# Kernel tuning notes

Hardware: AMD Instinct MI355X
Metric: run time of the kernel (lower is better)

Reference implementation:

```python
import jax, jax.numpy as jnp
import numpy as np

B, S, N, C, OUT = 16, 1024, 4096, 768, 256


def setup_inputs() -> dict:
    key = jax.random.key(0)
    k0, k1, k2, k3, k4 = jax.random.split(key, 5)
    seed_xyz = jax.random.normal(k0, (B, S, 3), jnp.float32)   # normalized seed coords
    p_last = jax.random.normal(k1, (B, N, 3), jnp.float32)     # lift3d last-stage coords
    f_last = jax.random.normal(k2, (B, C, N), jnp.float32)     # lift3d last-stage features (channel-first)
    W = jax.random.normal(k3, (OUT, C), jnp.float32) * 0.02    # Conv1d(C, 256, kernel_size=1) weight
    b = jax.random.normal(k4, (OUT,), jnp.float32) * 0.02      # Conv1d bias
    return {"seed_xyz": seed_xyz, "p_last": p_last, "f_last": f_last, "W": W, "b": b}


def reference(seed_xyz, p_last, f_last, W, b):
    # Squared pairwise distances [B,S,N] (argmin invariant to sqrt)
    d2 = (jnp.sum(seed_xyz * seed_xyz, axis=-1, keepdims=True)          # [B,S,1]
          - 2.0 * jnp.einsum('bsd,bnd->bsn', seed_xyz, p_last)          # [B,S,N]
          + jnp.sum(p_last * p_last, axis=-1)[:, None, :])              # [B,1,N]
    idx = jnp.argmin(d2, axis=-1)                                       # [B,S]
    # Gather nearest-neighbor features: [B,C,N] -> [B,C,S]
    gathered = jnp.take_along_axis(f_last, idx[:, None, :], axis=2)
    # 1x1 Conv1d projector: [B,C,S] x [OUT,C] -> [B,OUT,S]
    seed_features = jnp.einsum('bcs,oc->bos', gathered, W) + b[None, :, None]
    return seed_features
```

## Files before the change

### kernel.cpp

```cpp
#include <hip/hip_runtime.h>
#include <stdint.h>

#define B_   16
#define S_   1024
#define N_   4096
#define C_   768
#define OUT_ 256
#define NT_  (C_ / 32)

typedef short bf16x8 __attribute__((ext_vector_type(8)));
typedef short bf16x4 __attribute__((ext_vector_type(4)));
typedef float f32x4  __attribute__((ext_vector_type(4)));

#define GLOBAL_AS __attribute__((address_space(1)))
#define LDS_AS    __attribute__((address_space(3)))

__device__ __forceinline__ unsigned short f2bf(float f) {
    unsigned int u = __float_as_uint(f);
    u += 0x7fffu + ((u >> 16) & 1u);
    return (unsigned short)(u >> 16);
}

__device__ __forceinline__ void gl_lds16(const void* gsrc, void* ldst) {
    __builtin_amdgcn_global_load_lds((const GLOBAL_AS void*)gsrc,
                                     (LDS_AS void*)ldst, 16, 0, 0);
}

__global__ __launch_bounds__(256) void k_wconv(const float* __restrict__ W,
                                               unsigned short* __restrict__ Wb) {
    int i = (blockIdx.x * 256 + threadIdx.x) * 8;
    f32x4 a = *(const f32x4*)(W + i);
    f32x4 c = *(const f32x4*)(W + i + 4);
    bf16x8 o = {(short)f2bf(a[0]), (short)f2bf(a[1]),
                (short)f2bf(a[2]), (short)f2bf(a[3]),
                (short)f2bf(c[0]), (short)f2bf(c[1]),
                (short)f2bf(c[2]), (short)f2bf(c[3])};
    *(bf16x8*)(Wb + i) = o;
}

__global__ __launch_bounds__(256) void k_argmin(const float* __restrict__ seed,
                                                const float* __restrict__ pl,
                                                int* __restrict__ idx_out) {
    const int t    = threadIdx.x;
    const int lane = t & 63;
    const int w    = t >> 6;
    const int gw   = blockIdx.x * 4 + w;
    const int b    = gw >> 8;
    const int s0   = (gw & 255) * 4;

    float sx[4], sy[4], sz[4], s2[4], best[4];
    int   bidx[4];
#pragma unroll
    for (int j = 0; j < 4; ++j) {
        const float* sp = seed + (size_t)(b * S_ + s0 + j) * 3;
        sx[j] = sp[0]; sy[j] = sp[1]; sz[j] = sp[2];
        s2[j] = __fadd_rn(__fadd_rn(__fmul_rn(sx[j], sx[j]),
                                    __fmul_rn(sy[j], sy[j])),
                          __fmul_rn(sz[j], sz[j]));
        best[j] = 3.4e38f;
        bidx[j] = 0;
    }
    const float* pb = pl + (size_t)b * N_ * 3;

    for (int k = 0; k < N_ / 64; ++k) {
        const int   n  = k * 64 + lane;
        const float px = pb[n * 3 + 0];
        const float py = pb[n * 3 + 1];
        const float pz = pb[n * 3 + 2];
        const float p2 = __fadd_rn(__fadd_rn(__fmul_rn(px, px),
                                             __fmul_rn(py, py)),
                                   __fmul_rn(pz, pz));
#pragma unroll
        for (int j = 0; j < 4; ++j) {
            float dot = __fadd_rn(__fadd_rn(__fmul_rn(sx[j], px),
                                            __fmul_rn(sy[j], py)),
                                  __fmul_rn(sz[j], pz));
            float d2  = __fadd_rn(__fsub_rn(s2[j], __fmul_rn(2.0f, dot)), p2);
            if (d2 < best[j]) { best[j] = d2; bidx[j] = n; }
        }
    }

#pragma unroll
    for (int j = 0; j < 4; ++j) {
#pragma unroll
        for (int off = 32; off >= 1; off >>= 1) {
            float ob = __shfl_xor(best[j], off, 64);
            int   oi = __shfl_xor(bidx[j], off, 64);
            bool take = (ob < best[j]) || (ob == best[j] && oi < bidx[j]);
            if (take) { best[j] = ob; bidx[j] = oi; }
        }
        if (lane == 0) idx_out[b * S_ + s0 + j] = bidx[j];
    }
}

__global__ __launch_bounds__(256, 4) void k_pgemm(const float* __restrict__ f,
                                                  const unsigned short* __restrict__ Wb,
                                                  unsigned short* __restrict__ P) {
    __shared__ unsigned short ldsF[64 * 36];
    __shared__ unsigned short ldsW[256 * 32];
    const int t    = threadIdx.x;
    const int b    = blockIdx.x >> 6;
    const int nt   = blockIdx.x & 63;
    const int n0   = nt * 64;
    const int lane = t & 63;
    const int w    = t >> 6;
    const int quad = lane >> 4, l16 = lane & 15;

    f32x4 acc[4][4];
#pragma unroll
    for (int i = 0; i < 4; ++i)
#pragma unroll
        for (int j = 0; j < 4; ++j) acc[i][j] = (f32x4){0.f, 0.f, 0.f, 0.f};

    const int cb = t >> 4;
    const int nb = t & 15;
    const float* fB = f + (size_t)b * C_ * N_ + n0 + nb * 4;
    const unsigned short* wSrc = Wb + (size_t)(t >> 2) * C_ + (t & 3) * 8;

    for (int kt = 0; kt < NT_; ++kt) {
        const int k0 = kt * 32;
#pragma unroll
        for (int i = 0; i < 4; ++i)
            gl_lds16(wSrc + (size_t)i * 64 * C_ + k0, ldsW + i * 2048 + t * 8);
        f32x4 v0 = *(const f32x4*)(fB + (size_t)(k0 + cb * 2 + 0) * N_);
        f32x4 v1 = *(const f32x4*)(fB + (size_t)(k0 + cb * 2 + 1) * N_);
#pragma unroll
        for (int i = 0; i < 4; ++i) {
            unsigned int pk = (unsigned int)f2bf(v0[i]) |
                              ((unsigned int)f2bf(v1[i]) << 16);
            *(unsigned int*)(ldsF + (nb * 4 + i) * 36 + cb * 2) = pk;
        }
        __syncthreads();

        bf16x8 aF[4];
#pragma unroll
        for (int mi = 0; mi < 4; ++mi) {
            const unsigned short* p = ldsF + (mi * 16 + l16) * 36 + quad * 8;
            bf16x4 lo = *(const bf16x4*)p;
            bf16x4 hi = *(const bf16x4*)(p + 4);
            aF[mi] = __builtin_shufflevector(lo, hi, 0, 1, 2, 3, 4, 5, 6, 7);
        }
#pragma unroll
        for (int oi = 0; oi < 4; ++oi) {
            bf16x8 bF = *(const bf16x8*)(ldsW + (w * 64 + oi * 16 + l16) * 32 + quad * 8);
#pragma unroll
            for (int mi = 0; mi < 4; ++mi)
                acc[mi][oi] = __builtin_amdgcn_mfma_f32_16x16x32_bf16(
                    aF[mi], bF, acc[mi][oi], 0, 0, 0);
        }
        __syncthreads();
    }

    unsigned short* Pb = P + ((size_t)b * N_ + n0) * OUT_;
#pragma unroll
    for (int mi = 0; mi < 4; ++mi) {
#pragma unroll
        for (int r = 0; r < 4; ++r) {
            const int n = mi * 16 + quad * 4 + r;
            unsigned short* row = Pb + (size_t)n * OUT_;
#pragma unroll
            for (int oi = 0; oi < 4; ++oi) {
                const int o = w * 64 + oi * 16 + l16;
                row[o] = f2bf(acc[mi][oi][r]);
            }
        }
    }
}

__global__ __launch_bounds__(256) void k_out(const unsigned short* __restrict__ P,
                                             const int* __restrict__ idx,
                                             const float* __restrict__ bias,
                                             float* __restrict__ out) {
    __shared__ unsigned short tl[64 * 260];
    const int t  = threadIdx.x;
    const int b  = blockIdx.x >> 4;
    const int st = blockIdx.x & 15;
    const int s0 = st * 64;
    const unsigned short* Pb = P + (size_t)b * N_ * OUT_;

#pragma unroll
    for (int i = 0; i < 8; ++i) {
        const int g = i * 256 + t;
        const int s = g >> 5;
        const int p = g & 31;
        const int n = idx[b * S_ + s0 + s];
        const unsigned short* src = Pb + (size_t)n * OUT_ + p * 8;
        uint2 u0 = *(const uint2*)src;
        uint2 u1 = *(const uint2*)(src + 4);
        *(uint2*)(tl + s * 260 + p * 8)     = u0;
        *(uint2*)(tl + s * 260 + p * 8 + 4) = u1;
    }
    __syncthreads();

    const int lane = t & 63;
    const int w    = t >> 6;
    float* ob = out + (size_t)b * OUT_ * S_ + s0;
#pragma unroll 4
    for (int oo = 0; oo < 64; ++oo) {
        const int o = w * 64 + oo;
        const unsigned short u = tl[lane * 260 + o];
        const float val = __uint_as_float(((unsigned int)u) << 16) + bias[o];
        ob[(size_t)o * S_ + lane] = val;
    }
}

extern "C" void kernel_launch(void* const* d_in, const int* in_sizes, int n_in,
                              void* d_out, int out_size, void* d_ws, size_t ws_size,
                              hipStream_t stream) {
    const float* seed = (const float*)d_in[0];
    const float* pl   = (const float*)d_in[1];
    const float* f    = (const float*)d_in[2];
    const float* W    = (const float*)d_in[3];
    const float* bias = (const float*)d_in[4];
    float* out = (float*)d_out;

    int* idx            = (int*)d_ws;
    unsigned short* Wb  = (unsigned short*)((char*)d_ws + 65536);
    unsigned short* P   = (unsigned short*)((char*)d_ws + 524288);

    k_wconv <<<96,   256, 0, stream>>>(W, Wb);
    k_argmin<<<1024, 256, 0, stream>>>(seed, pl, idx);
    k_pgemm <<<1024, 256, 0, stream>>>(f, Wb, P);
    k_out   <<<256,  256, 0, stream>>>(P, idx, bias, out);
}
```

Before: 338.1 us.

## Fuse argmin into projection GEMM kernel and split gather kernel across output quarters

The nearest-neighbor argmin and the per-point projection GEMM now run as a single kernel, with each block first computing its argmin slice and then its GEMM tile. This removes one launch and the gap between the two kernels. The output gather kernel now launches four times as many blocks, each covering a quarter of the output channels with a smaller LDS tile, to improve occupancy and parallelism. The argmin phase still runs serially before the GEMM inside each block, so any overlap comes only from different blocks being in different phases.

```diff
diff --git a/kernel.cpp b/kernel.cpp
--- a/kernel.cpp
+++ b/kernel.cpp
@@ -38,130 +38,132 @@
     *(bf16x8*)(Wb + i) = o;
 }
 
-__global__ __launch_bounds__(256) void k_argmin(const float* __restrict__ seed,
-                                                const float* __restrict__ pl,
-                                                int* __restrict__ idx_out) {
+__global__ __launch_bounds__(256, 4) void k_fused2(const float* __restrict__ seed,
+                                                   const float* __restrict__ pl,
+                                                   int* __restrict__ idx_out,
+                                                   const float* __restrict__ f,
+                                                   const unsigned short* __restrict__ Wb,
+                                                   unsigned short* __restrict__ P) {
+    __shared__ unsigned short ldsF[64 * 36];
+    __shared__ unsigned short ldsW[256 * 32];
+    const int bid  = blockIdx.x;
     const int t    = threadIdx.x;
     const int lane = t & 63;
     const int w    = t >> 6;
-    const int gw   = blockIdx.x * 4 + w;
-    const int b    = gw >> 8;
-    const int s0   = (gw & 255) * 4;
-
-    float sx[4], sy[4], sz[4], s2[4], best[4];
-    int   bidx[4];
-#pragma unroll
-    for (int j = 0; j < 4; ++j) {
-        const float* sp = seed + (size_t)(b * S_ + s0 + j) * 3;
-        sx[j] = sp[0]; sy[j] = sp[1]; sz[j] = sp[2];
-        s2[j] = __fadd_rn(__fadd_rn(__fmul_rn(sx[j], sx[j]),
-                                    __fmul_rn(sy[j], sy[j])),
-                          __fmul_rn(sz[j], sz[j]));
-        best[j] = 3.4e38f;
-        bidx[j] = 0;
-    }
-    const float* pb = pl + (size_t)b * N_ * 3;
-
-    for (int k = 0; k < N_ / 64; ++k) {
-        const int   n  = k * 64 + lane;
-        const float px = pb[n * 3 + 0];
-        const float py = pb[n * 3 + 1];
-        const float pz = pb[n * 3 + 2];
-        const float p2 = __fadd_rn(__fadd_rn(__fmul_rn(px, px),
-                                             __fmul_rn(py, py)),
-                                   __fmul_rn(pz, pz));
+
+    {
+        const int gw = bid * 4 + w;
+        const int b  = gw >> 8;
+        const int s0 = (gw & 255) * 4;
+
+        float sx[4], sy[4], sz[4], s2[4], best[4];
+        int   bidx[4];
 #pragma unroll
         for (int j = 0; j < 4; ++j) {
-            float dot = __fadd_rn(__fadd_rn(__fmul_rn(sx[j], px),
-                                            __fmul_rn(sy[j], py)),
-                                  __fmul_rn(sz[j], pz));
-            float d2  = __fadd_rn(__fsub_rn(s2[j], __fmul_rn(2.0f, dot)), p2);
-            if (d2 < best[j]) { best[j] = d2; bidx[j] = n; }
-        }
-    }
-
-#pragma unroll
-    for (int j = 0; j < 4; ++j) {
-#pragma unroll
-        for (int off = 32; off >= 1; off >>= 1) {
-            float ob = __shfl_xor(best[j], off, 64);
-            int   oi = __shfl_xor(bidx[j], off, 64);
-            bool take = (ob < best[j]) || (ob == best[j] && oi < bidx[j]);
-            if (take) { best[j] = ob; bidx[j] = oi; }
-        }
-        if (lane == 0) idx_out[b * S_ + s0 + j] = bidx[j];
-    }
-}
-
-__global__ __launch_bounds__(256, 4) void k_pgemm(const float* __restrict__ f,
-                                                  const unsigned short* __restrict__ Wb,
-                                                  unsigned short* __restrict__ P) {
-    __shared__ unsigned short ldsF[64 * 36];
-    __shared__ unsigned short ldsW[256 * 32];
-    const int t    = threadIdx.x;
-    const int b    = blockIdx.x >> 6;
-    const int nt   = blockIdx.x & 63;
-    const int n0   = nt * 64;
-    const int lane = t & 63;
-    const int w    = t >> 6;
-    const int quad = lane >> 4, l16 = lane & 15;
-
-    f32x4 acc[4][4];
-#pragma unroll
-    for (int i = 0; i < 4; ++i)
-#pragma unroll
-        for (int j = 0; j < 4; ++j) acc[i][j] = (f32x4){0.f, 0.f, 0.f, 0.f};
-
-    const int cb = t >> 4;
-    const int nb = t & 15;
-    const float* fB = f + (size_t)b * C_ * N_ + n0 + nb * 4;
-    const unsigned short* wSrc = Wb + (size_t)(t >> 2) * C_ + (t & 3) * 8;
-
-    for (int kt = 0; kt < NT_; ++kt) {
-        const int k0 = kt * 32;
+            const float* sp = seed + (size_t)(b * S_ + s0 + j) * 3;
+            sx[j] = sp[0]; sy[j] = sp[1]; sz[j] = sp[2];
+            s2[j] = __fadd_rn(__fadd_rn(__fmul_rn(sx[j], sx[j]),
+                                        __fmul_rn(sy[j], sy[j])),
+                              __fmul_rn(sz[j], sz[j]));
+            best[j] = 3.4e38f;
+            bidx[j] = 0;
+        }
+        const float* pb = pl + (size_t)b * N_ * 3;
+
+        for (int k = 0; k < N_ / 64; ++k) {
+            const int   n  = k * 64 + lane;
+            const float px = pb[n * 3 + 0];
+            const float py = pb[n * 3 + 1];
+            const float pz = pb[n * 3 + 2];
+            const float p2 = __fadd_rn(__fadd_rn(__fmul_rn(px, px),
+                                                 __fmul_rn(py, py)),
+                                       __fmul_rn(pz, pz));
+#pragma unroll
+            for (int j = 0; j < 4; ++j) {
+                float dot = __fadd_rn(__fadd_rn(__fmul_rn(sx[j], px),
+                                                __fmul_rn(sy[j], py)),
+                                      __fmul_rn(sz[j], pz));
+                float d2  = __fadd_rn(__fsub_rn(s2[j], __fmul_rn(2.0f, dot)), p2);
+                if (d2 < best[j]) { best[j] = d2; bidx[j] = n; }
+            }
+        }
+
+#pragma unroll
+        for (int j = 0; j < 4; ++j) {
+#pragma unroll
+            for (int off = 32; off >= 1; off >>= 1) {
+                float ob = __shfl_xor(best[j], off, 64);
+                int   oi = __shfl_xor(bidx[j], off, 64);
+                bool take = (ob < best[j]) || (ob == best[j] && oi < bidx[j]);
+                if (take) { best[j] = ob; bidx[j] = oi; }
+            }
+            if (lane == 0) idx_out[b * S_ + s0 + j] = bidx[j];
+        }
+    }
+
+    {
+        const int b    = bid >> 6;
+        const int nt   = bid & 63;
+        const int n0   = nt * 64;
+        const int quad = lane >> 4, l16 = lane & 15;
+
+        f32x4 acc[4][4];
 #pragma unroll
         for (int i = 0; i < 4; ++i)
-            gl_lds16(wSrc + (size_t)i * 64 * C_ + k0, ldsW + i * 2048 + t * 8);
-        f32x4 v0 = *(const f32x4*)(fB + (size_t)(k0 + cb * 2 + 0) * N_);
-        f32x4 v1 = *(const f32x4*)(fB + (size_t)(k0 + cb * 2 + 1) * N_);
-#pragma unroll
-        for (int i = 0; i < 4; ++i) {
-            unsigned int pk = (unsigned int)f2bf(v0[i]) |
-                              ((unsigned int)f2bf(v1[i]) << 16);
-            *(unsigned int*)(ldsF + (nb * 4 + i) * 36 + cb * 2) = pk;
-        }
-        __syncthreads();
-
-        bf16x8 aF[4];
+#pragma unroll
+            for (int j = 0; j < 4; ++j) acc[i][j] = (f32x4){0.f, 0.f, 0.f, 0.f};
+
+        const int cb = t >> 4;
+        const int nb = t & 15;
+        const float* fB = f + (size_t)b * C_ * N_ + n0 + nb * 4;
+        const unsigned short* wSrc = Wb + (size_t)(t >> 2) * C_ + (t & 3) * 8;
+
+        for (int kt = 0; kt < NT_; ++kt) {
+            const int k0 = kt * 32;
+#pragma unroll
+            for (int i = 0; i < 4; ++i)
+                gl_lds16(wSrc + (size_t)i * 64 * C_ + k0, ldsW + i * 2048 + t * 8);
+            f32x4 v0 = *(const f32x4*)(fB + (size_t)(k0 + cb * 2 + 0) * N_);
+            f32x4 v1 = *(const f32x4*)(fB + (size_t)(k0 + cb * 2 + 1) * N_);
+#pragma unroll
+            for (int i = 0; i < 4; ++i) {
+                unsigned int pk = (unsigned int)f2bf(v0[i]) |
+                                  ((unsigned int)f2bf(v1[i]) << 16);
+                *(unsigned int*)(ldsF + (nb * 4 + i) * 36 + cb * 2) = pk;
+            }
+            __syncthreads();
+
+            bf16x8 aF[4];
+#pragma unroll
+            for (int mi = 0; mi < 4; ++mi) {
+                const unsigned short* p = ldsF + (mi * 16 + l16) * 36 + quad * 8;
+                bf16x4 lo = *(const bf16x4*)p;
+                bf16x4 hi = *(const bf16x4*)(p + 4);
+                aF[mi] = __builtin_shufflevector(lo, hi, 0, 1, 2, 3, 4, 5, 6, 7);
+            }
+#pragma unroll
+            for (int oi = 0; oi < 4; ++oi) {
+                bf16x8 bF = *(const bf16x8*)(ldsW + (w * 64 + oi * 16 + l16) * 32 + quad * 8);
+#pragma unroll
+                for (int mi = 0; mi < 4; ++mi)
+                    acc[mi][oi] = __builtin_amdgcn_mfma_f32_16x16x32_bf16(
+                        aF[mi], bF, acc[mi][oi], 0, 0, 0);
+            }
+            __syncthreads();
+        }
+
+        unsigned short* Pb = P + ((size_t)b * N_ + n0) * OUT_;
 #pragma unroll
         for (int mi = 0; mi < 4; ++mi) {
-            const unsigned short* p = ldsF + (mi * 16 + l16) * 36 + quad * 8;
-            bf16x4 lo = *(const bf16x4*)p;
-            bf16x4 hi = *(const bf16x4*)(p + 4);
-            aF[mi] = __builtin_shufflevector(lo, hi, 0, 1, 2, 3, 4, 5, 6, 7);
-        }
-#pragma unroll
-        for (int oi = 0; oi < 4; ++oi) {
-            bf16x8 bF = *(const bf16x8*)(ldsW + (w * 64 + oi * 16 + l16) * 32 + quad * 8);
-#pragma unroll
-            for (int mi = 0; mi < 4; ++mi)
-                acc[mi][oi] = __builtin_amdgcn_mfma_f32_16x16x32_bf16(
-                    aF[mi], bF, acc[mi][oi], 0, 0, 0);
-        }
-        __syncthreads();
-    }
-
-    unsigned short* Pb = P + ((size_t)b * N_ + n0) * OUT_;
-#pragma unroll
-    for (int mi = 0; mi < 4; ++mi) {
-#pragma unroll
-        for (int r = 0; r < 4; ++r) {
-            const int n = mi * 16 + quad * 4 + r;
-            unsigned short* row = Pb + (size_t)n * OUT_;
-#pragma unroll
-            for (int oi = 0; oi < 4; ++oi) {
-                const int o = w * 64 + oi * 16 + l16;
-                row[o] = f2bf(acc[mi][oi][r]);
+#pragma unroll
+            for (int r = 0; r < 4; ++r) {
+                const int n = mi * 16 + quad * 4 + r;
+                unsigned short* row = Pb + (size_t)n * OUT_;
+#pragma unroll
+                for (int oi = 0; oi < 4; ++oi) {
+                    const int o = w * 64 + oi * 16 + l16;
+                    row[o] = f2bf(acc[mi][oi][r]);
+                }
             }
         }
     }
@@ -171,24 +173,25 @@
                                              const int* __restrict__ idx,
                                              const float* __restrict__ bias,
                                              float* __restrict__ out) {
-    __shared__ unsigned short tl[64 * 260];
+    __shared__ unsigned short tl[64 * 68];
     const int t  = threadIdx.x;
-    const int b  = blockIdx.x >> 4;
-    const int st = blockIdx.x & 15;
+    const int b  = blockIdx.x >> 6;
+    const int st = (blockIdx.x >> 2) & 15;
+    const int oq = blockIdx.x & 3;
     const int s0 = st * 64;
     const unsigned short* Pb = P + (size_t)b * N_ * OUT_;
 
 #pragma unroll
-    for (int i = 0; i < 8; ++i) {
+    for (int i = 0; i < 2; ++i) {
         const int g = i * 256 + t;
-        const int s = g >> 5;
-        const int p = g & 31;
+        const int s = g >> 3;
+        const int p = g & 7;
         const int n = idx[b * S_ + s0 + s];
-        const unsigned short* src = Pb + (size_t)n * OUT_ + p * 8;
+        const unsigned short* src = Pb + (size_t)n * OUT_ + oq * 64 + p * 8;
         uint2 u0 = *(const uint2*)src;
         uint2 u1 = *(const uint2*)(src + 4);
-        *(uint2*)(tl + s * 260 + p * 8)     = u0;
-        *(uint2*)(tl + s * 260 + p * 8 + 4) = u1;
+        *(uint2*)(tl + s * 68 + p * 8)     = u0;
+        *(uint2*)(tl + s * 68 + p * 8 + 4) = u1;
     }
     __syncthreads();
 
@@ -196,9 +199,10 @@
     const int w    = t >> 6;
     float* ob = out + (size_t)b * OUT_ * S_ + s0;
 #pragma unroll 4
-    for (int oo = 0; oo < 64; ++oo) {
-        const int o = w * 64 + oo;
-        const unsigned short u = tl[lane * 260 + o];
+    for (int oo = 0; oo < 16; ++oo) {
+        const int col = w * 16 + oo;
+        const int o   = oq * 64 + col;
+        const unsigned short u = tl[lane * 68 + col];
         const float val = __uint_as_float(((unsigned int)u) << 16) + bias[o];
         ob[(size_t)o * S_ + lane] = val;
     }
@@ -219,7 +223,6 @@
     unsigned short* P   = (unsigned short*)((char*)d_ws + 524288);
 
     k_wconv <<<96,   256, 0, stream>>>(W, Wb);
-    k_argmin<<<1024, 256, 0, stream>>>(seed, pl, idx);
-    k_pgemm <<<1024, 256, 0, stream>>>(f, Wb, P);
-    k_out   <<<256,  256, 0, stream>>>(P, idx, bias, out);
-}
+    k_fused2<<<1024, 256, 0, stream>>>(seed, pl, idx, f, Wb, P);
+    k_out   <<<1024, 256, 0, stream>>>(P, idx, bias, out);
+}
```

Result: no change. 331.8 us (-1.9%).
